# Kernel optimization log

Hardware: AMD Instinct MI355X
Metric: run time of the kernel (lower is better)

## Reference

```python
import jax, jax.numpy as jnp
import numpy as np

SCALE = 2  # scale_factor; r = SCALE**2 must match kernels dim 2


def setup_inputs() -> dict:
    key = jax.random.key(0)
    k1, k2 = jax.random.split(key)
    burst = jax.random.normal(k1, (4, 8, 3, 128, 128), dtype=jnp.float32)
    # per-pixel adaptive kernels: (n, d, r, k, k, h, w), r = scale^2, k = 5
    kernels = jax.random.normal(k2, (4, 8, 4, 5, 5, 128, 128), dtype=jnp.float32)
    return {"burst": burst, "kernels": kernels}


def _adaptive_conv(burst, kernels):
    # burst: (n, d, c, h, w); kernels: (n, d, r, k, k, h, w)
    n, d, c, h, w = burst.shape
    k = kernels.shape[3]
    pad = k // 2
    padded = jnp.pad(burst, ((0, 0), (0, 0), (0, 0), (pad, pad), (pad, pad)))
    # gather kxk shifted windows -> (n, d, c, k, k, h, w); loop is over fixed k*k taps
    patches = jnp.stack(
        [jnp.stack([padded[..., i:i + h, j:j + w] for j in range(k)], axis=-3)
         for i in range(k)], axis=-4)
    # weighted sum over the kxk taps; burst channel c broadcasts against kernel r
    return jnp.einsum('ndcijhw,ndrijhw->ndcrhw', patches, kernels)


def _pixel_shuffle(x, s):
    # x: (n, d, c, r=s*s, h, w) -> (n, d, c, h*s, w*s), torch PixelShuffle order
    n, d, c, r, h, w = x.shape
    x = x.reshape(n, d, c, s, s, h, w)
    x = x.transpose(0, 1, 2, 5, 3, 6, 4)  # (n, d, c, h, s_i, w, s_j)
    return x.reshape(n, d, c, h * s, w * s)


def reference(burst, kernels):
    convolved = _adaptive_conv(burst, kernels)
    return _pixel_shuffle(convolved, SCALE)
```

## Files before the change

kernel.cpp:

```cpp
#include <hip/hip_runtime.h>

#define HH 128
#define WW 128
#define CC 3
#define RR 4
#define KK 5
#define ND 32
#define HW (HH * WW)

#define TROWS 12
#define TS    132
#define TSIZE (CC * TROWS * TS)

__global__ __launch_bounds__(256, 4) void adaptive_conv_ps(
    const float* __restrict__ burst,
    const float* __restrict__ kern,
    float* __restrict__ out)
{
    __shared__ float tile[TSIZE];

    const int tid = threadIdx.x;
    const int nd  = blockIdx.x >> 4;
    const int h0  = (blockIdx.x & 15) << 3;

    const float* bbase = burst + (size_t)nd * CC * HW;
    for (int idx = tid; idx < TSIZE; idx += 256) {
        int c   = idx / (TROWS * TS);
        int rem = idx - c * (TROWS * TS);
        int row = rem / TS;
        int col = rem - row * TS;
        int y = h0 - 2 + row;
        int x = col - 2;
        float v = 0.0f;
        if ((unsigned)y < (unsigned)HH && (unsigned)x < (unsigned)WW)
            v = bbase[c * HW + y * WW + x];
        tile[idx] = v;
    }
    __syncthreads();

    const int lrow = tid >> 5;
    const int w0   = (tid & 31) << 2;
    const int h    = h0 + lrow;

    const float* kbase = kern + (size_t)nd * RR * KK * KK * HW + h * WW + w0;

    float acc[CC][RR][4];
#pragma unroll
    for (int c = 0; c < CC; ++c)
#pragma unroll
        for (int r = 0; r < RR; ++r)
#pragma unroll
            for (int p = 0; p < 4; ++p)
                acc[c][r][p] = 0.0f;

    for (int i = 0; i < KK; ++i) {
        float rowv[CC][8];
#pragma unroll
        for (int c = 0; c < CC; ++c) {
            const float4* rp =
                (const float4*)&tile[c * TROWS * TS + (lrow + i) * TS + w0];
            *(float4*)&rowv[c][0] = rp[0];
            *(float4*)&rowv[c][4] = rp[1];
        }
#pragma unroll
        for (int j = 0; j < KK; ++j) {
            float kv[RR][4];
#pragma unroll
            for (int r = 0; r < RR; ++r)
                *(float4*)kv[r] =
                    *(const float4*)(kbase + (size_t)((r * KK + i) * KK + j) * HW);
#pragma unroll
            for (int c = 0; c < CC; ++c)
#pragma unroll
                for (int r = 0; r < RR; ++r)
#pragma unroll
                    for (int p = 0; p < 4; ++p)
                        acc[c][r][p] += kv[r][p] * rowv[c][j + p];
        }
    }

#pragma unroll
    for (int c = 0; c < CC; ++c) {
#pragma unroll
        for (int si = 0; si < 2; ++si) {
            float4 v0, v1;
            v0.x = acc[c][si * 2 + 0][0]; v0.y = acc[c][si * 2 + 1][0];
            v0.z = acc[c][si * 2 + 0][1]; v0.w = acc[c][si * 2 + 1][1];
            v1.x = acc[c][si * 2 + 0][2]; v1.y = acc[c][si * 2 + 1][2];
            v1.z = acc[c][si * 2 + 0][3]; v1.w = acc[c][si * 2 + 1][3];
            float* o = out + (((size_t)(nd * CC + c) * (2 * HH) + (2 * h + si)) * (2 * WW))
                           + 2 * w0;
            ((float4*)o)[0] = v0;
            ((float4*)o)[1] = v1;
        }
    }
}

extern "C" void kernel_launch(void* const* d_in, const int* in_sizes, int n_in,
                              void* d_out, int out_size, void* d_ws, size_t ws_size,
                              hipStream_t stream) {
    const float* burst = (const float*)d_in[0];
    const float* kern  = (const float*)d_in[1];
    float* out = (float*)d_out;

    adaptive_conv_ps<<<ND * 16, 256, 0, stream>>>(burst, kern, out);
}
```

Baseline: 325.0 us.

## Halve per-thread work and rows per block to double block count

Each block now covers 4 output rows instead of 8, and each thread computes 2 output pixels instead of 4, using float2 loads for the kernel weights and the shared tile. The grid doubles to 1024 blocks and the tap loop over i is fully unrolled. The aim is more waves and more outstanding memory requests to stream the large per-pixel kernel tensor at higher bandwidth. In exchange, the halo overhead in the shared tile rises and each thread has less reuse of the row data it reads.

```diff
diff --git a/kernel.cpp b/kernel.cpp
--- a/kernel.cpp
+++ b/kernel.cpp
@@ -8,7 +8,8 @@
 #define ND 32
 #define HW (HH * WW)
 
-#define TROWS 12
+#define ROWS_PER_BLK 4
+#define TROWS (ROWS_PER_BLK + 4)
 #define TS    132
 #define TSIZE (CC * TROWS * TS)
 
@@ -20,8 +21,8 @@
     __shared__ float tile[TSIZE];
 
     const int tid = threadIdx.x;
-    const int nd  = blockIdx.x >> 4;
-    const int h0  = (blockIdx.x & 15) << 3;
+    const int nd  = blockIdx.x >> 5;
+    const int h0  = (blockIdx.x & 31) * ROWS_PER_BLK;
 
     const float* bbase = burst + (size_t)nd * CC * HW;
     for (int idx = tid; idx < TSIZE; idx += 256) {
@@ -38,44 +39,46 @@
     }
     __syncthreads();
 
-    const int lrow = tid >> 5;
-    const int w0   = (tid & 31) << 2;
+    const int lrow = tid >> 6;
+    const int lane = tid & 63;
+    const int w0   = lane << 1;
     const int h    = h0 + lrow;
 
     const float* kbase = kern + (size_t)nd * RR * KK * KK * HW + h * WW + w0;
 
-    float acc[CC][RR][4];
+    float acc[CC][RR][2];
 #pragma unroll
     for (int c = 0; c < CC; ++c)
 #pragma unroll
-        for (int r = 0; r < RR; ++r)
+        for (int r = 0; r < RR; ++r) {
+            acc[c][r][0] = 0.0f;
+            acc[c][r][1] = 0.0f;
+        }
+
 #pragma unroll
-            for (int p = 0; p < 4; ++p)
-                acc[c][r][p] = 0.0f;
-
     for (int i = 0; i < KK; ++i) {
-        float rowv[CC][8];
+        float rowv[CC][6];
 #pragma unroll
         for (int c = 0; c < CC; ++c) {
-            const float4* rp =
-                (const float4*)&tile[c * TROWS * TS + (lrow + i) * TS + w0];
-            *(float4*)&rowv[c][0] = rp[0];
-            *(float4*)&rowv[c][4] = rp[1];
+            const float2* rp =
+                (const float2*)&tile[c * TROWS * TS + (lrow + i) * TS + w0];
+            *(float2*)&rowv[c][0] = rp[0];
+            *(float2*)&rowv[c][2] = rp[1];
+            *(float2*)&rowv[c][4] = rp[2];
         }
 #pragma unroll
         for (int j = 0; j < KK; ++j) {
-            float kv[RR][4];
+            float2 kv[RR];
 #pragma unroll
             for (int r = 0; r < RR; ++r)
-                *(float4*)kv[r] =
-                    *(const float4*)(kbase + (size_t)((r * KK + i) * KK + j) * HW);
+                kv[r] = *(const float2*)(kbase + (size_t)((r * KK + i) * KK + j) * HW);
 #pragma unroll
             for (int c = 0; c < CC; ++c)
 #pragma unroll
-                for (int r = 0; r < RR; ++r)
-#pragma unroll
-                    for (int p = 0; p < 4; ++p)
-                        acc[c][r][p] += kv[r][p] * rowv[c][j + p];
+                for (int r = 0; r < RR; ++r) {
+                    acc[c][r][0] += kv[r].x * rowv[c][j + 0];
+                    acc[c][r][1] += kv[r].y * rowv[c][j + 1];
+                }
         }
     }
 
@@ -83,15 +86,14 @@
     for (int c = 0; c < CC; ++c) {
 #pragma unroll
         for (int si = 0; si < 2; ++si) {
-            float4 v0, v1;
-            v0.x = acc[c][si * 2 + 0][0]; v0.y = acc[c][si * 2 + 1][0];
-            v0.z = acc[c][si * 2 + 0][1]; v0.w = acc[c][si * 2 + 1][1];
-            v1.x = acc[c][si * 2 + 0][2]; v1.y = acc[c][si * 2 + 1][2];
-            v1.z = acc[c][si * 2 + 0][3]; v1.w = acc[c][si * 2 + 1][3];
+            float4 v;
+            v.x = acc[c][si * 2 + 0][0];
+            v.y = acc[c][si * 2 + 1][0];
+            v.z = acc[c][si * 2 + 0][1];
+            v.w = acc[c][si * 2 + 1][1];
             float* o = out + (((size_t)(nd * CC + c) * (2 * HH) + (2 * h + si)) * (2 * WW))
                            + 2 * w0;
-            ((float4*)o)[0] = v0;
-            ((float4*)o)[1] = v1;
+            *(float4*)o = v;
         }
     }
 }
@@ -103,5 +105,5 @@
     const float* kern  = (const float*)d_in[1];
     float* out = (float*)d_out;
 
-    adaptive_conv_ps<<<ND * 16, 256, 0, stream>>>(burst, kern, out);
+    adaptive_conv_ps<<<ND * 32, 256, 0, stream>>>(burst, kern, out);
 }
```

Result: faster. 315.8 us (-2.8%).
